# Performance work log

Measured on AMD Instinct MI355X. Metric: run time of the kernel, lower is better.

## Reference

```python
import jax, jax.numpy as jnp
import numpy as np
from jax.scipy.special import gammaln

REG = 0.1  # reg_param from __init__


def setup_inputs() -> dict:
    key = jax.random.key(0)
    k1, k2 = jax.random.split(key)
    D, C, S, Q = 512, 64, 16, 2048  # feature_dim, n_way, shots, n_query
    X_support = jax.random.normal(k1, (C * S, D), dtype=jnp.float32)
    # balanced class labels (equivalent to argmax of a one-hot y)
    labels = jnp.arange(C * S, dtype=jnp.int32) % C
    X_query = jax.random.normal(k2, (Q, D), dtype=jnp.float32)
    # learned parameters, initialized exactly as in the torch module
    m = jnp.zeros((1, D), dtype=jnp.float32)
    kappa = jnp.asarray(0.1, dtype=jnp.float32)
    nu = jnp.asarray(float(D), dtype=jnp.float32)
    triu_diag = jnp.ones((D,), dtype=jnp.float32)
    triu_lower = jnp.eye(D, dtype=jnp.float32)
    return {"X_support": X_support, "labels": labels, "X_query": X_query,
            "m": m, "kappa": kappa, "nu": nu,
            "triu_diag": triu_diag, "triu_lower": triu_lower, "n_classes": 64}


def _forward(X_support, X_query, m, kappa, nu, triu_diag, triu_lower, labels, n_classes):
    N, D = X_support.shape
    C = int(n_classes)
    S = N // C  # balanced episode: N_j == S for every class

    # lower_triu = diag(|triu_diag|) + triu_lower * strictly_lower_mask
    mask = jnp.tril(jnp.ones((D, D), dtype=X_support.dtype), -1)
    L = jnp.diag(jnp.abs(triu_diag)) + triu_lower * mask

    kap = jnp.abs(kappa) + 1e-6
    nu_ = jnp.clip(nu, D - 1 + 1e-6)

    # group support samples by class: [C, S, D] (stable sort keeps per-class order)
    order = jnp.argsort(labels)
    Xg = X_support[order].reshape(C, S, D)
    Xmean = Xg.mean(axis=1)  # [C, D]

    # posterior means mu_j = kappa/(kappa+N) m + N/(kappa+N) mean(X_j)
    mu = (kap / (kap + S)) * m + (S / (kap + S)) * Xmean  # [C, D]

    # sum_outer(X_j) as one batched GEMM instead of a per-row loop
    XtX = jnp.einsum('csd,cse->cde', Xg, Xg)  # [C, D, D]
    base = L @ L.T + kap * (m.T @ m)          # [D, D], shared across classes
    S_ns = base[None] + XtX - (kap + S) * jnp.einsum('cd,ce->cde', mu, mu)
    sigma = S_ns * ((kap + S + 1.0) / ((nu_ + S - D + 1.0) * (kap + S)))  # [C, D, D]

    eye = jnp.eye(D, dtype=sigma.dtype)
    sigma_inv = (1.0 - REG) * jnp.linalg.inv(sigma) + REG * eye  # regularize()

    common = nu_ + S + 1.0 - D  # scalar (equal shots per class)
    _, logdet = jnp.linalg.slogdet(sigma)  # [C]
    bias = (gammaln(0.5 * (common + D)) - gammaln(0.5 * common)
            - 0.5 * D * jnp.log(common) - 0.5 * logdet)  # [C]

    # batched Mahalanobis distances: replaces nested python loops in predict()
    diff = X_query[None, :, :] - mu[:, None, :]              # [C, Q, D]
    t = jnp.einsum('cqd,cde->cqe', diff, sigma_inv)          # [C, Q, D]
    dist = jnp.sum(t * diff, axis=-1)                        # [C, Q]

    logits = bias[:, None] - 0.5 * (common + D) * jnp.log1p(dist / common)
    return logits.T  # [Q, C]


def reference(X_support, labels, X_query, m, kappa, nu, triu_diag, triu_lower, n_classes):
    return _forward(X_support, X_query, m, kappa, nu, triu_diag, triu_lower,
                    labels, n_classes)
```

## Files before the change

### kernel.cpp

```cpp
#include <hip/hip_runtime.h>
#include <math.h>

#define DD    512
#define CNUM  64
#define SHOTS 16
#define NSUP  1024
#define QNQ   2048
#define REGP  0.1f
#define XKS   4

typedef __attribute__((ext_vector_type(8))) short short8;
typedef __attribute__((ext_vector_type(4))) float f32x4;

__device__ __forceinline__ unsigned short f2bf(float f) {
  unsigned int u = __float_as_uint(f);
  unsigned int r = (u + 0x7fffu + ((u >> 16) & 1u)) >> 16;
  return (unsigned short)r;
}
__device__ __forceinline__ float bf2f(unsigned short h) {
  return __uint_as_float((unsigned int)h << 16);
}

static constexpr size_t OFF_W     = 0;
static constexpr size_t OFF_MU    = OFF_W     + 512*512;
static constexpr size_t OFF_Y     = OFF_MU    + 64*512;
static constexpr size_t OFF_Z     = OFF_Y     + 3136*512;
static constexpr size_t OFF_WM    = OFF_Z     + 3136;
static constexpr size_t OFF_CONST = OFF_WM    + 512;
static constexpr size_t OFF_IDX   = OFF_CONST + 16;
static constexpr size_t OFF_RMAP  = OFF_IDX   + 1024;
static constexpr size_t OFF_ZG    = OFF_RMAP  + 1088;
static constexpr size_t OFF_VMU   = OFF_ZG    + 1088;
static constexpr size_t OFF_MUBMU = OFF_VMU   + 1088;
static constexpr size_t OFF_MUN   = OFF_MUBMU + 64;
static constexpr size_t OFF_MINV  = OFF_MUN   + 64;
static constexpr size_t OFF_BIAS  = OFF_MINV  + 64*289;
static constexpr size_t OFF_QNRM  = OFF_BIAS  + 64;
static constexpr size_t OFF_YN    = OFF_QNRM  + 2048;
static constexpr size_t OFF_XMU   = OFF_YN    + 2048;
static constexpr size_t OFF_RG    = OFF_XMU   + (size_t)XKS*2048*64;
static constexpr size_t OFF_P     = OFF_RG    + 1088*2048;
static constexpr size_t OFF_PX    = OFF_P     + 3136*512;
static constexpr size_t OFF_PW    = OFF_PX    + 3136*512;


__device__ __forceinline__ void px_rows(const float* __restrict__ Xq,
    const float* __restrict__ Xs, unsigned short* __restrict__ PX, int r0) {
  int tid = threadIdx.x;
  int row = r0 + (tid >> 6), lane = tid & 63;
  const float* src = (row < QNQ) ? Xq + (size_t)row * DD
                                 : Xs + (size_t)(row - QNQ) * DD;
  size_t prow = (size_t)row * 1024;
  #pragma unroll
  for (int p = 0; p < 2; p++) {
    int col = lane * 8 + p * 4;
    float4 v = *(const float4*)(src + col);
    ushort4 hi, lo;
    hi.x = f2bf(v.x); lo.x = f2bf(v.x - bf2f(hi.x));
    hi.y = f2bf(v.y); lo.y = f2bf(v.y - bf2f(hi.y));
    hi.z = f2bf(v.z); lo.z = f2bf(v.z - bf2f(hi.z));
    hi.w = f2bf(v.w); lo.w = f2bf(v.w - bf2f(hi.w));
    *(ushort4*)(PX + prow + col) = hi;
    *(ushort4*)(PX + prow + 512 + col) = lo;
  }
}

__global__ __launch_bounds__(256) void f_init(const float* tdiag, const float* tlow,
    const float* kappa, const float* nu, const int* labels, const float* Xs,
    const float* Xq, const float* m, float* W, float* cst, int* idx,
    int* rowmap, float* mu, float* mun,
    unsigned short* PX, unsigned short* PW) {
  __shared__ float sh[2 * 64 * 68 + 32 * 33];
  __shared__ int sidx[SHOTS];
  int b = blockIdx.x, tid = threadIdx.x;
  if (b < 8) {
    int jb = b;
    float* Ld = sh;
    float* Wd = sh + 64 * 68;
    float* tsh = sh + 2 * 64 * 68;
    for (int t = tid; t < 4096; t += 256) {
      int r = t >> 6, c = t & 63;
      int gr = jb * 64 + r;
      float v = (r == c) ? fabsf(tdiag[gr])
              : (r > c ? tlow[(size_t)gr * DD + jb * 64 + c] : 0.0f);
      Ld[r * 68 + c] = v;
      Wd[r * 68 + c] = 0.0f;
    }
    __syncthreads();
    if (tid < 64) {
      int s = tid >> 4, t = tid & 15;
      int r0 = s * 16;
      #pragma unroll
      for (int i = 0; i < 16; i++) {
        float w = (i == t) ? 1.0f : 0.0f;
        #pragma unroll
        for (int k = 0; k < 16; k++)
          if (k < i) w -= Ld[(r0 + i) * 68 + r0 + k] * Wd[(r0 + k) * 68 + r0 + t];
        Wd[(r0 + i) * 68 + r0 + t] = w / Ld[(r0 + i) * 68 + r0 + i];
      }
    }
    __syncthreads();
    for (int g2 = 0; g2 < 2; g2++) {
      int r0 = g2 * 32 + 16, c0 = g2 * 32;
      int rr = tid >> 4, cc = tid & 15;
      float t_ = 0.0f;
      #pragma unroll
      for (int k = 0; k < 16; k++)
        t_ += Ld[(r0 + rr) * 68 + c0 + k] * Wd[(c0 + k) * 68 + c0 + cc];
      tsh[rr * 33 + cc] = t_;
      __syncthreads();
      float x = 0.0f;
      #pragma unroll
      for (int k = 0; k < 16; k++)
        x -= Wd[(r0 + rr) * 68 + r0 + k] * tsh[k * 33 + cc];
      Wd[(r0 + rr) * 68 + c0 + cc] = x;
      __syncthreads();
    }
    {
      int rr = tid >> 6, cc = tid & 63;
      #pragma unroll
      for (int p = 0; p < 4; p++) {
        int r = rr + p * 4, c = cc;
        if (c < 32) {
          float t_ = 0.0f;
          #pragma unroll
          for (int k = 0; k < 32; k++)
            t_ += Ld[(32 + r) * 68 + k] * Wd[k * 68 + c];
          tsh[r * 33 + c] = t_;
        } else {
          int c2 = c - 32;
          float t_ = 0.0f;
          #pragma unroll
          for (int k = 0; k < 32; k++)
            t_ += Ld[(32 + r + 16) * 68 + k] * Wd[k * 68 + c2];
          tsh[(r + 16) * 33 + c2] = t_;
        }
      }
      __syncthreads();
      #pragma unroll
      for (int p = 0; p < 4; p++) {
        int r = rr + p * 4, c = cc;
        int r2 = (c < 32) ? r : r + 16;
        int c2 = (c < 32) ? c : c - 32;
        float x = 0.0f;
        #pragma unroll
        for (int k = 0; k < 32; k++)
          x -= Wd[(32 + r2) * 68 + 32 + k] * tsh[k * 33 + c2];
        Wd[(32 + r2) * 68 + c2] = x;
      }
    }
    __syncthreads();
    float* Wblk = W + (size_t)(jb * 64) * DD + jb * 64;
    for (int t = tid; t < 4096; t += 256) {
      int r = t >> 6, c = t & 63;
      float v = Wd[r * 68 + c];
      Wblk[(size_t)r * DD + c] = v;
      unsigned short h = f2bf(v), l = f2bf(v - bf2f(h));
      size_t prow = (size_t)(jb * 64 + r) * 1024 + jb * 64 + c;
      PW[prow] = h;
      PW[prow + 512] = l;
    }
  } else if (b == 8) {
    if (tid == 0) {
      float kap = fabsf(kappa[0]) + 1e-6f;
      float nu_ = fmaxf(nu[0], (float)(DD - 1) + 1e-6f);
      float common = nu_ + (float)SHOTS + 1.0f - (float)DD;
      float scale = (kap + SHOTS + 1.0f) / ((nu_ + SHOTS - DD + 1.0f) * (kap + SHOTS));
      cst[0] = kap;
      cst[1] = scale;
      cst[2] = common;
      cst[3] = 0.5f * (common + DD);
      cst[4] = lgammaf(0.5f * (common + DD)) - lgammaf(0.5f * common)
               - 0.5f * (float)DD * logf(common);
      cst[5] = -(kap + SHOTS);
      cst[6] = kap / (kap + SHOTS);
      cst[7] = 1.0f / (kap + SHOTS);
      cst[8] = (float)DD * logf(scale);
      cst[9] = -1.0f / (kap + SHOTS);
    }
  } else if (b < 73) {
    int c = b - 9;
    if (tid < 64) {
      int lane = tid, cnt = 0;
      for (int i0 = 0; i0 < NSUP; i0 += 64) {
        int lab = labels[i0 + lane];
        unsigned long long mm = __ballot(lab == c);
        if (lab == c) {
          int pos = cnt + __popcll(mm & ((1ull << lane) - 1ull));
          if (pos < SHOTS) idx[c * SHOTS + pos] = i0 + lane;
        }
        cnt += __popcll(mm);
      }
    }
    __syncthreads();
    if (tid < 17)
      rowmap[c * 17 + tid] = (tid < SHOTS) ? (QNQ + idx[c * SHOTS + tid])
                                           : (QNQ + NSUP + c);
  } else {
    int c = b - 73;
    if (tid < 64) {
      int lane = tid, cnt = 0;
      for (int i0 = 0; i0 < NSUP; i0 += 64) {
        int lab = labels[i0 + lane];
        unsigned long long mm = __ballot(lab == c);
        if (lab == c) {
          int pos = cnt + __popcll(mm & ((1ull << lane) - 1ull));
          if (pos < SHOTS) sidx[pos] = i0 + lane;
        }
        cnt += __popcll(mm);
      }
    }
    __syncthreads();
    float kap = fabsf(kappa[0]) + 1e-6f;
    float cm = kap / (kap + SHOTS), cx = 1.0f / (kap + SHOTS);
    float* red = sh;
    float acc = 0.0f;
    size_t prow = (size_t)(3072 + c) * 1024;
    for (int d = tid; d < DD; d += 256) {
      float s = 0.0f;
      for (int sh_ = 0; sh_ < SHOTS; sh_++)
        s += Xs[(size_t)sidx[sh_] * DD + d];
      float v = cm * m[d] + cx * s;
      mu[(size_t)c * DD + d] = v;
      unsigned short h = f2bf(v), l = f2bf(v - bf2f(h));
      PX[prow + d] = h;
      PX[prow + 512 + d] = l;
      acc += v * v;
    }
    red[tid] = acc;
    __syncthreads();
    for (int off = 128; off > 0; off >>= 1) {
      if (tid < off) red[tid] += red[tid + off];
      __syncthreads();
    }
    if (tid == 0) mun[c] = red[0];
  }
}

__device__ __forceinline__ void tile_stage(float* S, const float* __restrict__ G, int ldg) {
  int tid = threadIdx.x;
  #pragma unroll
  for (int p = 0; p < 4; p++) {
    int f4 = tid + 256 * p;
    int row = f4 >> 4, c4 = (f4 & 15) * 4;
    *(float4*)&S[row * 68 + c4] = *(const float4*)(G + (size_t)row * ldg + c4);
  }
}
__device__ __forceinline__ void tile_fma(float acc[4][4], const float* As, const float* Bs) {
  int tid = threadIdx.x, tr = tid >> 4, tc = tid & 15;
  #pragma unroll
  for (int kk = 0; kk < 64; kk++) {
    float a[4];
    #pragma unroll
    for (int x = 0; x < 4; x++) a[x] = As[(tr * 4 + x) * 68 + kk];
    float4 bv = *(const float4*)&Bs[kk * 68 + tc * 4];
    float bb[4] = {bv.x, bv.y, bv.z, bv.w};
    #pragma unroll
    for (int x = 0; x < 4; x++)
      #pragma unroll
      for (int y = 0; y < 4; y++) acc[x][y] += a[x] * bb[y];
  }
}
__device__ __forceinline__ void tile_out_neg(const float acc[4][4], float* W,
    unsigned short* PW, int gr0, int gc0) {
  int tid = threadIdx.x, tr = tid >> 4, tc = tid & 15;
  #pragma unroll
  for (int x = 0; x < 4; x++) {
    #pragma unroll
    for (int y = 0; y < 4; y++) {
      float v = -acc[x][y];
      W[(size_t)(gr0 + tr * 4 + x) * DD + gc0 + tc * 4 + y] = v;
      unsigned short h = f2bf(v), l = f2bf(v - bf2f(h));
      size_t prow = (size_t)(gr0 + tr * 4 + x) * 1024 + gc0 + tc * 4 + y;
      PW[prow] = h;
      PW[prow + 512] = l;
    }
  }
}

#define GBK 16
__global__ __launch_bounds__(256) void k_m128_xmu(const float* __restrict__ tlow,
    const float* __restrict__ W_, float* __restrict__ Wout,
    const float* __restrict__ Xq, const float* __restrict__ Mu,
    float* __restrict__ xmup, unsigned short* __restrict__ PW) {
  __shared__ float sh[3 * 64 * 68];
  int b = blockIdx.x, tid = threadIdx.x;
  if (b < 4) {
    float* As = sh;
    float* Bs = sh + 64 * 68;
    float* tsh = sh + 2 * 64 * 68;
    int base = b * 128;
    float tacc[4][4] = {};
    tile_stage(As, tlow + (size_t)(base + 64) * DD + base, DD);
    tile_stage(Bs, W_ + (size_t)base * DD + base, DD);
    __syncthreads();
    tile_fma(tacc, As, Bs);
    __syncthreads();
    {
      int tr = tid >> 4, tc = tid & 15;
      #pragma unroll
      for (int x = 0; x < 4; x++)
        #pragma unroll
        for (int y = 0; y < 4; y++) tsh[(tr * 4 + x) * 68 + tc * 4 + y] = tacc[x][y];
    }
    tile_stage(As, W_ + (size_t)(base + 64) * DD + base + 64, DD);
    __syncthreads();
    float xacc[4][4] = {};
    tile_fma(xacc, As, tsh);
    tile_out_neg(xacc, Wout, PW, base + 64, base);
  } else {
    float* Ms = sh;
    float* Qs = sh + 64 * 68;
    int xb = b - 4;
    int bm = (xb & 63) * 32, kq = xb >> 6;
    int tr = tid >> 4, tc = tid & 15;
    float acc[4][2] = {};
    int k0s = kq * (DD / XKS), k0e = k0s + DD / XKS;
    for (int k0 = k0s; k0 < k0e; k0 += GBK) {
      {
        int row = tid >> 2, k4 = tid & 3;
        float4 v = *(const float4*)(Mu + (size_t)row * DD + k0 + k4 * 4);
        Ms[(k4 * 4 + 0) * 68 + row] = v.x; Ms[(k4 * 4 + 1) * 68 + row] = v.y;
        Ms[(k4 * 4 + 2) * 68 + row] = v.z; Ms[(k4 * 4 + 3) * 68 + row] = v.w;
      }
      if (tid < 128) {
        int row = tid >> 2, k4 = tid & 3;
        float4 v = *(const float4*)(Xq + (size_t)(bm + row) * DD + k0 + k4 * 4);
        Qs[(k4 * 4 + 0) * 36 + row] = v.x; Qs[(k4 * 4 + 1) * 36 + row] = v.y;
        Qs[(k4 * 4 + 2) * 36 + row] = v.z; Qs[(k4 * 4 + 3) * 36 + row] = v.w;
      }
      __syncthreads();
      #pragma unroll
      for (int kk = 0; kk < GBK; kk++) {
        float4 m0 = *(const float4*)&Ms[kk * 68 + tr * 4];
        float a[4] = {m0.x, m0.y, m0.z, m0.w};
        float q0 = Qs[kk * 36 + tc * 2], q1 = Qs[kk * 36 + tc * 2 + 1];
        #pragma unroll
        for (int y = 0; y < 4; y++) {
          acc[y][0] += a[y] * q0;
          acc[y][1] += a[y] * q1;
        }
      }
      __syncthreads();
    }
    #pragma unroll
    for (int y = 0; y < 4; y++) {
      float2 v = make_float2(acc[y][0], acc[y][1]);
      *(float2*)(xmup + ((size_t)kq * CNUM + tr * 4 + y) * QNQ + bm + tc * 2) = v;
    }
  }
}

__global__ __launch_bounds__(256) void k_m256(const float* __restrict__ tlow,
    float* __restrict__ W, unsigned short* __restrict__ PW,
    const float* __restrict__ Xq, const float* __restrict__ Xs,
    unsigned short* __restrict__ PX) {
  __shared__ float sh[3 * 64 * 68];
  int b = blockIdx.x, tid = threadIdx.x;
  if (b >= 8) { px_rows(Xq, Xs, PX, (b - 8) * 4); return; }
  float* As = sh;
  float* Bs = sh + 64 * 68;
  float* tsh = sh + 2 * 64 * 68;
  int g = b >> 2, rem = b & 3, i = rem >> 1, j = rem & 1;
  int base = g * 256;
  float xacc[4][4] = {};
  for (int k = 0; k <= i; k++) {
    float tacc[4][4] = {};
    for (int l = j; l < 2; l++) {
      __syncthreads();
      tile_stage(As, tlow + (size_t)(base + 128 + 64 * k) * DD + base + 64 * l, DD);
      tile_stage(Bs, W + (size_t)(base + 64 * l) * DD + base + 64 * j, DD);
      __syncthreads();
      tile_fma(tacc, As, Bs);
    }
    __syncthreads();
    {
      int tr = tid >> 4, tc = tid & 15;
      #pragma unroll
      for (int x = 0; x < 4; x++)
        #pragma unroll
        for (int y = 0; y < 4; y++) tsh[(tr * 4 + x) * 68 + tc * 4 + y] = tacc[x][y];
    }
    tile_stage(As, W + (size_t)(base + 128 + 64 * i) * DD + base + 128 + 64 * k, DD);
    __syncthreads();
    tile_fma(xacc, As, tsh);
  }
  tile_out_neg(xacc, W, PW, base + 128 + 64 * i, base + 64 * j);
}

__device__ __forceinline__ void nn64_sh(float* As, float* Bs,
    const float* __restrict__ A, int lda, const float* __restrict__ B, int ldb,
    float* __restrict__ Cd, int ldc, int k0, int k1, float sgn,
    unsigned short* __restrict__ Pw, int gr0, int gc0) {
  int tid = threadIdx.x, tr = tid >> 4, tc = tid & 15;
  float acc[4][4] = {};
  for (int kc = k0; kc < k1; kc += 64) {
    #pragma unroll
    for (int p = 0; p < 4; p++) {
      int f4 = tid + 256 * p;
      int row = f4 >> 4, c4 = f4 & 15;
      *(float4*)&As[row * 68 + c4 * 4] = *(const float4*)(A + (size_t)row * lda + kc + c4 * 4);
      *(float4*)&Bs[row * 68 + c4 * 4] = *(const float4*)(B + (size_t)(kc + row) * ldb + c4 * 4);
    }
    __syncthreads();
    #pragma unroll
    for (int kk = 0; kk < 64; kk++) {
      float a[4];
      #pragma unroll
      for (int x = 0; x < 4; x++) a[x] = As[(tr * 4 + x) * 68 + kk];
      float4 bv = *(const float4*)&Bs[kk * 68 + tc * 4];
      float bb[4] = {bv.x, bv.y, bv.z, bv.w};
      #pragma unroll
      for (int x = 0; x < 4; x++)
        #pragma unroll
        for (int y = 0; y < 4; y++) acc[x][y] += a[x] * bb[y];
    }
    __syncthreads();
  }
  #pragma unroll
  for (int x = 0; x < 4; x++) {
    float4 v = make_float4(sgn * acc[x][0], sgn * acc[x][1],
                           sgn * acc[x][2], sgn * acc[x][3]);
    *(float4*)(Cd + (size_t)(tr * 4 + x) * ldc + tc * 4) = v;
    if (Pw) {
      size_t prow = (size_t)(gr0 + tr * 4 + x) * 1024 + gc0 + tc * 4;
      float vv[4] = {v.x, v.y, v.z, v.w};
      #pragma unroll
      for (int y = 0; y < 4; y++) {
        unsigned short h = f2bf(vv[y]), l = f2bf(vv[y] - bf2f(h));
        Pw[prow + y] = h;
        Pw[prow + 512 + y] = l;
      }
    }
  }
}

__global__ __launch_bounds__(256) void k_triT(const float* __restrict__ tlow,
                                              const float* __restrict__ W,
                                              float* __restrict__ T,
                                              const float* __restrict__ Xq,
                                              const float* __restrict__ Xs,
                                              unsigned short* __restrict__ PX) {
  __shared__ float sh[2 * 64 * 68];
  int b = blockIdx.x;
  if (b >= 16) { px_rows(Xq, Xs, PX, 1024 + (b - 16) * 4); return; }
  int ti = b >> 2, tj = b & 3;
  const float* A = tlow + (size_t)(256 + ti * 64) * DD;
  const float* B = W + (size_t)tj * 64;
  float* Cd = T + (size_t)(ti * 64) * 256 + tj * 64;
  nn64_sh(sh, sh + 64 * 68, A, DD, B, DD, Cd, 256, tj * 64, 256, 1.0f, nullptr, 0, 0);
}

__global__ __launch_bounds__(256) void k_triX(float* __restrict__ W,
                                              const float* __restrict__ T,
                                              unsigned short* __restrict__ PW,
                                              const float* __restrict__ Xq,
                                              const float* __restrict__ Xs,
                                              unsigned short* __restrict__ PX) {
  __shared__ float sh[2 * 64 * 68];
  int b = blockIdx.x;
  if (b >= 16) { px_rows(Xq, Xs, PX, 2048 + (b - 16) * 4); return; }
  int ti = b >> 2, tj = b & 3;
  const float* A = W + (size_t)(256 + ti * 64) * DD + 256;
  const float* B = T + tj * 64;
  int gr0 = 256 + ti * 64, gc0 = tj * 64;
  float* Cd = W + (size_t)gr0 * DD + gc0;
  nn64_sh(sh, sh + 64 * 68, A, DD, B, 256, Cd, DD, 0, (ti + 1) * 64, -1.0f, PW, gr0, gc0);
}

#define PSTR 72
__global__ __launch_bounds__(256) void f_y_wm(const unsigned short* __restrict__ PX,
    const unsigned short* __restrict__ PW, const float* __restrict__ W,
    const float* __restrict__ m, float* __restrict__ Y,
    unsigned short* __restrict__ Pm, float* __restrict__ wm) {
  __shared__ unsigned short AshH[64 * PSTR];
  __shared__ unsigned short AshL[64 * PSTR];
  __shared__ unsigned short BshH[64 * PSTR];
  __shared__ unsigned short BshL[64 * PSTR];
  int b = blockIdx.x, tid = threadIdx.x;
  if (b < 392) {
    int mt = b >> 3, nt = b & 7;
    int bm = mt * 64, bn = nt * 64;
    int lane = tid & 63, wave = tid >> 6;
    int wr = wave >> 1, wc = wave & 1;
    int mrow = lane & 15, q = lane >> 4;
    f32x4 acc00 = {}, acc01 = {}, acc10 = {}, acc11 = {};
    int kchunks = nt + 1;
    for (int it = 0; it < kchunks; it++) {
      int kc = it * 64;
      #pragma unroll
      for (int p = 0; p < 2; p++) {
        int idx = tid + 256 * p;
        int row = idx >> 3, c8 = (idx & 7) * 8;
        *(short8*)&AshH[row * PSTR + c8] =
            *(const short8*)(PX + (size_t)(bm + row) * 1024 + kc + c8);
        *(short8*)&AshL[row * PSTR + c8] =
            *(const short8*)(PX + (size_t)(bm + row) * 1024 + 512 + kc + c8);
        *(short8*)&BshH[row * PSTR + c8] =
            *(const short8*)(PW + (size_t)(bn + row) * 1024 + kc + c8);
        *(short8*)&BshL[row * PSTR + c8] =
            *(const short8*)(PW + (size_t)(bn + row) * 1024 + 512 + kc + c8);
      }
      __syncthreads();
      #pragma unroll
      for (int ks = 0; ks < 2; ks++) {
        int ko = ks * 32 + q * 8;
        short8 ah0 = *(const short8*)&AshH[(wr * 32 + mrow) * PSTR + ko];
        short8 ah1 = *(const short8*)&AshH[(wr * 32 + 16 + mrow) * PSTR + ko];
        short8 al0 = *(const short8*)&AshL[(wr * 32 + mrow) * PSTR + ko];
        short8 al1 = *(const short8*)&AshL[(wr * 32 + 16 + mrow) * PSTR + ko];
        short8 bh0 = *(const short8*)&BshH[(wc * 32 + mrow) * PSTR + ko];
        short8 bh1 = *(const short8*)&BshH[(wc * 32 + 16 + mrow) * PSTR + ko];
        short8 bl0 = *(const short8*)&BshL[(wc * 32 + mrow) * PSTR + ko];
        short8 bl1 = *(const short8*)&BshL[(wc * 32 + 16 + mrow) * PSTR + ko];
        acc00 = __builtin_amdgcn_mfma_f32_16x16x32_bf16(ah0, bh0, acc00, 0, 0, 0);
        acc00 = __builtin_amdgcn_mfma_f32_16x16x32_bf16(ah0, bl0, acc00, 0, 0, 0);
        acc00 = __builtin_amdgcn_mfma_f32_16x16x32_bf16(al0, bh0, acc00, 0, 0, 0);
        acc01 = __builtin_amdgcn_mfma_f32_16x16x32_bf16(ah0, bh1, acc01, 0, 0, 0);
        acc01 = __builtin_amdgcn_mfma_f32_16x16x32_bf16(ah0, bl1, acc01, 0, 0, 0);
        acc01 = __builtin_amdgcn_mfma_f32_16x16x32_bf16(al0, bh1, acc01, 0, 0, 0);
        acc10 = __builtin_amdgcn_mfma_f32_16x16x32_bf16(ah1, bh0, acc10, 0, 0, 0);
        acc10 = __builtin_amdgcn_mfma_f32_16x16x32_bf16(ah1, bl0, acc10, 0, 0, 0);
        acc10 = __builtin_amdgcn_mfma_f32_16x16x32_bf16(al1, bh0, acc10, 0, 0, 0);
        acc11 = __builtin_amdgcn_mfma_f32_16x16x32_bf16(ah1, bh1, acc11, 0, 0, 0);
        acc11 = __builtin_amdgcn_mfma_f32_16x16x32_bf16(ah1, bl1, acc11, 0, 0, 0);
        acc11 = __builtin_amdgcn_mfma_f32_16x16x32_bf16(al1, bh1, acc11, 0, 0, 0);
      }
      __syncthreads();
    }
    #pragma unroll
    for (int r = 0; r < 4; r++) {
      int row0 = bm + wr * 32 + q * 4 + r;
      int row1 = row0 + 16;
      int col0 = bn + wc * 32 + mrow;
      float vv[4] = {acc00[r], acc01[r], acc10[r], acc11[r]};
      int rows[4] = {row0, row0, row1, row1};
      int cols[4] = {col0, col0 + 16, col0, col0 + 16};
      #pragma unroll
      for (int e = 0; e < 4; e++) {
        Y[(size_t)rows[e] * DD + cols[e]] = vv[e];
        unsigned short h = f2bf(vv[e]), l = f2bf(vv[e] - bf2f(h));
        Pm[(size_t)rows[e] * 1024 + cols[e]] = h;
        Pm[(size_t)rows[e] * 1024 + 512 + cols[e]] = l;
      }
    }
  } else {
    int wave = tid >> 6, lane = tid & 63;
    int row = (b - 392) * 4 + wave;
    float s = 0.0f;
    for (int j = lane; j <= row; j += 64) s += W[(size_t)row * DD + j] * m[j];
    for (int off = 32; off > 0; off >>= 1) s += __shfl_down(s, off);
    if (lane == 0) wm[row] = s;
  }
}

__global__ __launch_bounds__(256) void f_z_rg_gram(const unsigned short* __restrict__ Pm,
    const float* __restrict__ Y, const float* __restrict__ tdiag,
    const int* __restrict__ rowmap, const float* __restrict__ Xq,
    const float* __restrict__ wm, float* __restrict__ cst,
    float* __restrict__ Rg,
    float* __restrict__ z, float* __restrict__ qn, float* __restrict__ yn,
    float* __restrict__ zg, float* __restrict__ Vmu, float* __restrict__ muBmu,
    float* __restrict__ Minv, float* __restrict__ bias) {
  __shared__ float sh[9216];
  __shared__ float csmS;
  int b = blockIdx.x, tid = threadIdx.x;
  if (b < 64) {
    int c = b;
    int lane = tid & 63, wave = tid >> 6;
    float* Ys  = sh;
    float* aug = sh + 8772;
    float* zsv = aug + 306;
    float kap = cst[0], cst9 = cst[9];
    for (int t = tid; t < 17 * 128; t += 256) {
      int r = t >> 7, col = t & 127;
      *(float4*)&Ys[r * 516 + col * 4] =
          *(const float4*)(Y + (size_t)rowmap[c * 17 + r] * DD + col * 4);
    }
    float ldb_r = 0.0f;
    if (wave == 0) {
      float aa = 0.0f, ll = 0.0f;
      for (int t = lane; t < DD; t += 64) {
        float w = wm[t]; aa += w * w;
        ll += logf(fabsf(tdiag[t]));
      }
      #pragma unroll
      for (int off = 32; off > 0; off >>= 1) {
        aa += __shfl_xor(aa, off);
        ll += __shfl_xor(ll, off);
      }
      ldb_r = 2.0f * ll + logf(1.0f + kap * aa);
      if (lane == 0) csmS = kap / (1.0f + kap * aa);
    }
    __syncthreads();
    if (wave > 0) {
      for (int a = wave - 1; a < 17; a += 3) {
        float s = 0.0f;
        for (int j = lane; j < 128; j += 64) {
          float4 yv = *(const float4*)&Ys[a * 516 + j * 4];
          float4 wv = *(const float4*)(wm + j * 4);
          s += yv.x * wv.x + yv.y * wv.y + yv.z * wv.z + yv.w * wv.w;
        }
        #pragma unroll
        for (int off = 32; off > 0; off >>= 1) s += __shfl_xor(s, off);
        if (lane == 0) zsv[a] = s;
      }
    }
    __syncthreads();
    float csm = csmS;
    for (int e = tid; e < 153; e += 256) {
      int a = (int)((sqrtf(8.0f * (float)e + 1.0f) - 1.0f) * 0.5f);
      while (((a + 1) * (a + 2)) / 2 <= e) a++;
      while ((a * (a + 1)) / 2 > e) a--;
      int bb = e - (a * (a + 1)) / 2;
      const float* ra = &Ys[a * 516];
      const float* rb = &Ys[bb * 516];
      float s = 0.0f;
      for (int k = 0; k < 128; k++) {
        float4 va = *(const float4*)&ra[k * 4];
        float4 vb = *(const float4*)&rb[k * 4];
        s += va.x * vb.x + va.y * vb.y + va.z * vb.z + va.w * vb.w;
      }
      float g = s - csm * zsv[a] * zsv[bb];
      if (a == bb) g += (a < 16) ? 1.0f : cst9;
      aug[a * 18 + bb] = g;
      if (a != bb) aug[bb * 18 + a] = g;
    }
    __syncthreads();
    if (wave == 0) {
      float colv[17];
      bool left = lane < 17;
      bool right = (lane >= 17 && lane < 34);
      #pragma unroll
      for (int r = 0; r < 17; r++) {
        float lv = aug[r * 18 + (lane & 31)];
        colv[r] = left ? lv : ((right && (lane - 17) == r) ? 1.0f : 0.0f);
      }
      float det = 0.0f;
      #pragma unroll
      for (int k = 0; k < 17; k++) {
        float best = fabsf(colv[k]); int bp = k;
        #pragma unroll
        for (int r = k + 1; r < 17; r++) {
          float v = fabsf(colv[r]);
          if (v > best) { best = v; bp = r; }
        }
        int p = __shfl(bp, k);
        float pv = colv[k];
        #pragma unroll
        for (int r = k + 1; r < 17; r++) pv = (p == r) ? colv[r] : pv;
        float oldk = colv[k];
        #pragma unroll
        for (int r = k + 1; r < 17; r++) colv[r] = (p == r) ? oldk : colv[r];
        colv[k] = pv;
        float piv = __shfl(pv, k);
        if (lane == 0) det += logf(fabsf(piv));
        float invp = 1.0f / piv;
        float rk = pv * invp;
        colv[k] = rk;
        #pragma unroll
        for (int r = 0; r < 17; r++) {
          if (r == k) continue;
          float ck = __shfl(colv[r], k);
          colv[r] = fmaf(-ck, rk, colv[r]);
        }
      }
      if (right) {
        int bb = lane - 17;
        #pragma unroll
        for (int r = 0; r < 17; r++)
          Minv[(size_t)c * 289 + r * 17 + bb] = colv[r];
      }
      if (lane == 0) {
        float slog = logf(fabsf(cst[5])) + det;
        float logdetSigma = cst[8] + ldb_r + slog;
        bias[c] = cst[4] - 0.5f * logdetSigma;
      }
    } else if (wave == 1) {
      if (lane < 17) {
        float gv = aug[lane * 18 + 16];
        if (lane == 16) gv -= cst9;
        Vmu[c * 17 + lane] = gv;
        if (lane == 16) muBmu[c] = gv;
        zg[c * 17 + lane] = zsv[lane];
      }
    }
  } else if (b == 64) {
    if (tid < 64) {
      float aa = 0.0f, ll = 0.0f;
      for (int t = tid; t < DD; t += 64) {
        float w = wm[t]; aa += w * w;
        ll += logf(fabsf(tdiag[t]));
      }
      #pragma unroll
      for (int off = 32; off > 0; off >>= 1) {
        aa += __shfl_xor(aa, off);
        ll += __shfl_xor(ll, off);
      }
      if (tid == 0) {
        float kap = cst[0];
        cst[10] = kap / (1.0f + kap * aa);
        cst[11] = 2.0f * ll + logf(1.0f + kap * aa);
      }
    }
  } else if (b < 609) {
    unsigned short* ush = (unsigned short*)sh;
    unsigned short* AH = ush;
    unsigned short* AL = ush + 64 * PSTR;
    unsigned short* BH = ush + 2 * 64 * PSTR;
    unsigned short* BL = ush + 3 * 64 * PSTR;
    int rb = b - 65;
    int bm = (rb >> 5) * 64, bn = (rb & 31) * 64;
    int lane = tid & 63, wave = tid >> 6;
    int wr = wave >> 1, wc = wave & 1;
    int mrow = lane & 15, q = lane >> 4;
    int srowA[2];
    #pragma unroll
    for (int p = 0; p < 2; p++) srowA[p] = rowmap[bm + ((tid + 256 * p) >> 3)];
    f32x4 acc00 = {}, acc01 = {}, acc10 = {}, acc11 = {};
    for (int it = 0; it < 8; it++) {
      int kc = it * 64;
      #pragma unroll
      for (int p = 0; p < 2; p++) {
        int idx = tid + 256 * p;
        int row = idx >> 3, c8 = (idx & 7) * 8;
        *(short8*)&AH[row * PSTR + c8] =
            *(const short8*)(Pm + (size_t)srowA[p] * 1024 + kc + c8);
        *(short8*)&AL[row * PSTR + c8] =
            *(const short8*)(Pm + (size_t)srowA[p] * 1024 + 512 + kc + c8);
        *(short8*)&BH[row * PSTR + c8] =
            *(const short8*)(Pm + (size_t)(bn + row) * 1024 + kc + c8);
        *(short8*)&BL[row * PSTR + c8] =
            *(const short8*)(Pm + (size_t)(bn + row) * 1024 + 512 + kc + c8);
      }
      __syncthreads();
      #pragma unroll
      for (int ks = 0; ks < 2; ks++) {
        int ko = ks * 32 + q * 8;
        short8 ah0 = *(const short8*)&AH[(wr * 32 + mrow) * PSTR + ko];
        short8 ah1 = *(const short8*)&AH[(wr * 32 + 16 + mrow) * PSTR + ko];
        short8 al0 = *(const short8*)&AL[(wr * 32 + mrow) * PSTR + ko];
        short8 al1 = *(const short8*)&AL[(wr * 32 + 16 + mrow) * PSTR + ko];
        short8 bh0 = *(const short8*)&BH[(wc * 32 + mrow) * PSTR + ko];
        short8 bh1 = *(const short8*)&BH[(wc * 32 + 16 + mrow) * PSTR + ko];
        short8 bl0 = *(const short8*)&BL[(wc * 32 + mrow) * PSTR + ko];
        short8 bl1 = *(const short8*)&BL[(wc * 32 + 16 + mrow) * PSTR + ko];
        acc00 = __builtin_amdgcn_mfma_f32_16x16x32_bf16(ah0, bh0, acc00, 0, 0, 0);
        acc00 = __builtin_amdgcn_mfma_f32_16x16x32_bf16(ah0, bl0, acc00, 0, 0, 0);
        acc00 = __builtin_amdgcn_mfma_f32_16x16x32_bf16(al0, bh0, acc00, 0, 0, 0);
        acc01 = __builtin_amdgcn_mfma_f32_16x16x32_bf16(ah0, bh1, acc01, 0, 0, 0);
        acc01 = __builtin_amdgcn_mfma_f32_16x16x32_bf16(ah0, bl1, acc01, 0, 0, 0);
        acc01 = __builtin_amdgcn_mfma_f32_16x16x32_bf16(al0, bh1, acc01, 0, 0, 0);
        acc10 = __builtin_amdgcn_mfma_f32_16x16x32_bf16(ah1, bh0, acc10, 0, 0, 0);
        acc10 = __builtin_amdgcn_mfma_f32_16x16x32_bf16(ah1, bl0, acc10, 0, 0, 0);
        acc10 = __builtin_amdgcn_mfma_f32_16x16x32_bf16(al1, bh0, acc10, 0, 0, 0);
        acc11 = __builtin_amdgcn_mfma_f32_16x16x32_bf16(ah1, bh1, acc11, 0, 0, 0);
        acc11 = __builtin_amdgcn_mfma_f32_16x16x32_bf16(ah1, bl1, acc11, 0, 0, 0);
        acc11 = __builtin_amdgcn_mfma_f32_16x16x32_bf16(al1, bh1, acc11, 0, 0, 0);
      }
      __syncthreads();
    }
    #pragma unroll
    for (int r = 0; r < 4; r++) {
      int row0 = bm + wr * 32 + q * 4 + r;
      int row1 = row0 + 16;
      int col0 = bn + wc * 32 + mrow;
      Rg[(size_t)row0 * QNQ + col0]      = acc00[r];
      Rg[(size_t)row0 * QNQ + col0 + 16] = acc01[r];
      Rg[(size_t)row1 * QNQ + col0]      = acc10[r];
      Rg[(size_t)row1 * QNQ + col0 + 16] = acc11[r];
    }
  } else {
    int wave = tid >> 6, lane = tid & 63;
    int row = (b - 609) * 4 + wave;
    const float* xr = Xq + (size_t)row * DD;
    const float* yr = Y + (size_t)row * DD;
    float sz = 0.0f, s1 = 0.0f, s2 = 0.0f;
    for (int j4 = lane; j4 < 128; j4 += 64) {
      float4 xv = *(const float4*)(xr + j4 * 4);
      float4 yv = *(const float4*)(yr + j4 * 4);
      float4 wv = *(const float4*)(wm + j4 * 4);
      sz += yv.x * wv.x + yv.y * wv.y + yv.z * wv.z + yv.w * wv.w;
      s1 += xv.x * xv.x + xv.y * xv.y + xv.z * xv.z + xv.w * xv.w;
      s2 += yv.x * yv.x + yv.y * yv.y + yv.z * yv.z + yv.w * yv.w;
    }
    for (int off = 32; off > 0; off >>= 1) {
      sz += __shfl_down(sz, off);
      s1 += __shfl_down(s1, off);
      s2 += __shfl_down(s2, off);
    }
    if (lane == 0) {
      z[row] = sz;
      qn[row] = s1;
      yn[row] = s2;
    }
  }
}

__global__ __launch_bounds__(256) void k_logits(const float* __restrict__ Rg,
    const float* z, const float* zg,
    const float* Vmu, const float* muBmu, const float* mun, const float* yn,
    const float* qn, const float* xmup, const float* Minv, const float* bias,
    const float* cst, float* out) {
  __shared__ float Ms[289], Vs[17], Zs[17];
  int c = blockIdx.y;
  int q = blockIdx.x * 256 + threadIdx.x;
  for (int t = threadIdx.x; t < 289; t += 256) Ms[t] = Minv[(size_t)c * 289 + t];
  if (threadIdx.x < 17) {
    Vs[threadIdx.x] = Vmu[c * 17 + threadIdx.x];
    Zs[threadIdx.x] = zg[c * 17 + threadIdx.x];
  }
  __syncthreads();
  float csm = cst[10], scale = cst[1], common = cst[2], coef = cst[3];
  float zq = z[q];
  float r[17];
  float xBmu = 0.0f;
  for (int a = 0; a < 17; a++) {
    float raw = Rg[(size_t)(c * 17 + a) * QNQ + q] - csm * Zs[a] * zq;
    if (a == 16) xBmu = raw;
    r[a] = raw - Vs[a];
  }
  float qB = yn[q] - csm * zq * zq;
  float quadB = qB - 2.0f * xBmu + muBmu[c];
  float corr = 0.0f;
  for (int a = 0; a < 17; a++) {
    float e = 0.0f;
    for (int bb = 0; bb < 17; bb++) e += Ms[a * 17 + bb] * r[bb];
    corr += r[a] * e;
  }
  float distB = (quadB - corr) / scale;
  float xm = 0.0f;
  #pragma unroll
  for (int p = 0; p < XKS; p++)
    xm += xmup[((size_t)(p * CNUM + c)) * QNQ + q];
  float dn = qn[q] - 2.0f * xm + mun[c];
  float dist = (1.0f - REGP) * distB + REGP * dn;
  out[(size_t)q * CNUM + c] = bias[c] - coef * log1pf(dist / common);
}

extern "C" void kernel_launch(void* const* d_in, const int* in_sizes, int n_in,
                              void* d_out, int out_size, void* d_ws, size_t ws_size,
                              hipStream_t stream) {
  const float* Xs    = (const float*)d_in[0];
  const int*   labels= (const int*)d_in[1];
  const float* Xq    = (const float*)d_in[2];
  const float* m     = (const float*)d_in[3];
  const float* kappa = (const float*)d_in[4];
  const float* nu    = (const float*)d_in[5];
  const float* tdiag = (const float*)d_in[6];
  const float* tlow  = (const float*)d_in[7];
  float* ws = (float*)d_ws;
  float* W    = ws + OFF_W;
  float* mu   = ws + OFF_MU;
  float* Y    = ws + OFF_Y;
  float* z    = ws + OFF_Z;
  float* wm   = ws + OFF_WM;
  float* cst  = ws + OFF_CONST;
  int*   idx  = (int*)(ws + OFF_IDX);
  int*   rmap = (int*)(ws + OFF_RMAP);
  float* zg   = ws + OFF_ZG;
  float* Vmu  = ws + OFF_VMU;
  float* muBmu= ws + OFF_MUBMU;
  float* mun  = ws + OFF_MUN;
  float* Minv = ws + OFF_MINV;
  float* bias = ws + OFF_BIAS;
  float* qn   = ws + OFF_QNRM;
  float* yn   = ws + OFF_YN;
  float* xmup = ws + OFF_XMU;
  float* Rg   = ws + OFF_RG;
  unsigned short* P  = (unsigned short*)(ws + OFF_P);
  unsigned short* PX = (unsigned short*)(ws + OFF_PX);
  unsigned short* PW = (unsigned short*)(ws + OFF_PW);
  float* Ttmp = ws + OFF_RG;
  float* out  = (float*)d_out;

  f_init<<<137, 256, 0, stream>>>(tdiag, tlow, kappa, nu, labels, Xs, Xq, m,
                                  W, cst, idx, rmap, mu, mun, PX, PW);
  k_m128_xmu<<<260, 256, 0, stream>>>(tlow, W, W, Xq, mu, xmup, PW);
  k_m256<<<8 + 256, 256, 0, stream>>>(tlow, W, PW, Xq, Xs, PX);
  k_triT<<<16 + 256, 256, 0, stream>>>(tlow, W, Ttmp, Xq, Xs, PX);
  k_triX<<<16 + 256, 256, 0, stream>>>(W, Ttmp, PW, Xq, Xs, PX);
  f_y_wm<<<520, 256, 0, stream>>>(PX, PW, W, m, Y, P, wm);
  f_z_rg_gram<<<64 + 1 + 544 + 512, 256, 0, stream>>>(P, Y, tdiag, rmap, Xq, wm,
                                                      cst, Rg, z, qn, yn,
                                                      zg, Vmu, muBmu, Minv, bias);
  k_logits<<<dim3(QNQ / 256, CNUM), 256, 0, stream>>>(Rg, z, zg, Vmu, muBmu,
                                                      mun, yn, qn, xmup, Minv, bias,
                                                      cst, out);
  (void)in_sizes; (void)n_in; (void)out_size; (void)ws_size;
}
```

Measured before the change: 187.5 us.

## Fuse two-pass triangular inverse block update into one kernel, widen xmu K-tile

The two kernels that computed the 256x256 off-diagonal block of the triangular inverse (first T = L21*W11 into a scratch buffer, then W21 = -W22*T) become one kernel. Each block now recomputes the needed T tiles in shared memory and accumulates the product directly. This removes a launch and the global round trip through the temporary, at the cost of redundant T-tile computation across blocks. The diff also keeps the 16x16 forward-substitution column in registers instead of shared memory, and doubles the K step of the query-mean product to cut loop iterations and barriers.

```diff
diff --git a/kernel.cpp b/kernel.cpp
--- a/kernel.cpp
+++ b/kernel.cpp
@@ -90,14 +90,17 @@
     if (tid < 64) {
       int s = tid >> 4, t = tid & 15;
       int r0 = s * 16;
+      float wreg[16];
       #pragma unroll
       for (int i = 0; i < 16; i++) {
         float w = (i == t) ? 1.0f : 0.0f;
         #pragma unroll
         for (int k = 0; k < 16; k++)
-          if (k < i) w -= Ld[(r0 + i) * 68 + r0 + k] * Wd[(r0 + k) * 68 + r0 + t];
-        Wd[(r0 + i) * 68 + r0 + t] = w / Ld[(r0 + i) * 68 + r0 + i];
-      }
+          if (k < i) w -= Ld[(r0 + i) * 68 + r0 + k] * wreg[k];
+        wreg[i] = w / Ld[(r0 + i) * 68 + r0 + i];
+      }
+      #pragma unroll
+      for (int i = 0; i < 16; i++) Wd[(r0 + i) * 68 + r0 + t] = wreg[i];
     }
     __syncthreads();
     for (int g2 = 0; g2 < 2; g2++) {
@@ -278,7 +281,7 @@
   }
 }
 
-#define GBK 16
+#define GBK 32
 __global__ __launch_bounds__(256) void k_m128_xmu(const float* __restrict__ tlow,
     const float* __restrict__ W_, float* __restrict__ Wout,
     const float* __restrict__ Xq, const float* __restrict__ Mu,
@@ -317,14 +320,16 @@
     float acc[4][2] = {};
     int k0s = kq * (DD / XKS), k0e = k0s + DD / XKS;
     for (int k0 = k0s; k0 < k0e; k0 += GBK) {
-      {
-        int row = tid >> 2, k4 = tid & 3;
+      #pragma unroll
+      for (int p = 0; p < 2; p++) {
+        int idx = tid + 256 * p;
+        int row = idx >> 3, k4 = idx & 7;
         float4 v = *(const float4*)(Mu + (size_t)row * DD + k0 + k4 * 4);
         Ms[(k4 * 4 + 0) * 68 + row] = v.x; Ms[(k4 * 4 + 1) * 68 + row] = v.y;
         Ms[(k4 * 4 + 2) * 68 + row] = v.z; Ms[(k4 * 4 + 3) * 68 + row] = v.w;
       }
-      if (tid < 128) {
-        int row = tid >> 2, k4 = tid & 3;
+      {
+        int row = tid >> 3, k4 = tid & 7;
         float4 v = *(const float4*)(Xq + (size_t)(bm + row) * DD + k0 + k4 * 4);
         Qs[(k4 * 4 + 0) * 36 + row] = v.x; Qs[(k4 * 4 + 1) * 36 + row] = v.y;
         Qs[(k4 * 4 + 2) * 36 + row] = v.z; Qs[(k4 * 4 + 3) * 36 + row] = v.w;
@@ -388,84 +393,40 @@
   tile_out_neg(xacc, W, PW, base + 128 + 64 * i, base + 64 * j);
 }
 
-__device__ __forceinline__ void nn64_sh(float* As, float* Bs,
-    const float* __restrict__ A, int lda, const float* __restrict__ B, int ldb,
-    float* __restrict__ Cd, int ldc, int k0, int k1, float sgn,
-    unsigned short* __restrict__ Pw, int gr0, int gc0) {
-  int tid = threadIdx.x, tr = tid >> 4, tc = tid & 15;
-  float acc[4][4] = {};
-  for (int kc = k0; kc < k1; kc += 64) {
-    #pragma unroll
-    for (int p = 0; p < 4; p++) {
-      int f4 = tid + 256 * p;
-      int row = f4 >> 4, c4 = f4 & 15;
-      *(float4*)&As[row * 68 + c4 * 4] = *(const float4*)(A + (size_t)row * lda + kc + c4 * 4);
-      *(float4*)&Bs[row * 68 + c4 * 4] = *(const float4*)(B + (size_t)(kc + row) * ldb + c4 * 4);
-    }
-    __syncthreads();
-    #pragma unroll
-    for (int kk = 0; kk < 64; kk++) {
-      float a[4];
-      #pragma unroll
-      for (int x = 0; x < 4; x++) a[x] = As[(tr * 4 + x) * 68 + kk];
-      float4 bv = *(const float4*)&Bs[kk * 68 + tc * 4];
-      float bb[4] = {bv.x, bv.y, bv.z, bv.w};
+__global__ __launch_bounds__(256) void k_tri512(const float* __restrict__ tlow,
+    float* __restrict__ W, unsigned short* __restrict__ PW,
+    const float* __restrict__ Xq, const float* __restrict__ Xs,
+    unsigned short* __restrict__ PX) {
+  __shared__ float sh[3 * 64 * 68];
+  int b = blockIdx.x, tid = threadIdx.x;
+  if (b >= 16) { px_rows(Xq, Xs, PX, 1024 + (b - 16) * 4); return; }
+  float* As = sh;
+  float* Bs = sh + 64 * 68;
+  float* tsh = sh + 2 * 64 * 68;
+  int ti = b >> 2, tj = b & 3;
+  float xacc[4][4] = {};
+  for (int k = 0; k <= ti; k++) {
+    float tacc[4][4] = {};
+    for (int l = tj; l < 4; l++) {
+      __syncthreads();
+      tile_stage(As, tlow + (size_t)(256 + k * 64) * DD + l * 64, DD);
+      tile_stage(Bs, W + (size_t)(l * 64) * DD + tj * 64, DD);
+      __syncthreads();
+      tile_fma(tacc, As, Bs);
+    }
+    __syncthreads();
+    {
+      int tr = tid >> 4, tc = tid & 15;
       #pragma unroll
       for (int x = 0; x < 4; x++)
         #pragma unroll
-        for (int y = 0; y < 4; y++) acc[x][y] += a[x] * bb[y];
-    }
-    __syncthreads();
-  }
-  #pragma unroll
-  for (int x = 0; x < 4; x++) {
-    float4 v = make_float4(sgn * acc[x][0], sgn * acc[x][1],
-                           sgn * acc[x][2], sgn * acc[x][3]);
-    *(float4*)(Cd + (size_t)(tr * 4 + x) * ldc + tc * 4) = v;
-    if (Pw) {
-      size_t prow = (size_t)(gr0 + tr * 4 + x) * 1024 + gc0 + tc * 4;
-      float vv[4] = {v.x, v.y, v.z, v.w};
-      #pragma unroll
-      for (int y = 0; y < 4; y++) {
-        unsigned short h = f2bf(vv[y]), l = f2bf(vv[y] - bf2f(h));
-        Pw[prow + y] = h;
-        Pw[prow + 512 + y] = l;
-      }
-    }
-  }
-}
-
-__global__ __launch_bounds__(256) void k_triT(const float* __restrict__ tlow,
-                                              const float* __restrict__ W,
-                                              float* __restrict__ T,
-                                              const float* __restrict__ Xq,
-                                              const float* __restrict__ Xs,
-                                              unsigned short* __restrict__ PX) {
-  __shared__ float sh[2 * 64 * 68];
-  int b = blockIdx.x;
-  if (b >= 16) { px_rows(Xq, Xs, PX, 1024 + (b - 16) * 4); return; }
-  int ti = b >> 2, tj = b & 3;
-  const float* A = tlow + (size_t)(256 + ti * 64) * DD;
-  const float* B = W + (size_t)tj * 64;
-  float* Cd = T + (size_t)(ti * 64) * 256 + tj * 64;
-  nn64_sh(sh, sh + 64 * 68, A, DD, B, DD, Cd, 256, tj * 64, 256, 1.0f, nullptr, 0, 0);
-}
-
-__global__ __launch_bounds__(256) void k_triX(float* __restrict__ W,
-                                              const float* __restrict__ T,
-                                              unsigned short* __restrict__ PW,
-                                              const float* __restrict__ Xq,
-                                              const float* __restrict__ Xs,
-                                              unsigned short* __restrict__ PX) {
-  __shared__ float sh[2 * 64 * 68];
-  int b = blockIdx.x;
-  if (b >= 16) { px_rows(Xq, Xs, PX, 2048 + (b - 16) * 4); return; }
-  int ti = b >> 2, tj = b & 3;
-  const float* A = W + (size_t)(256 + ti * 64) * DD + 256;
-  const float* B = T + tj * 64;
-  int gr0 = 256 + ti * 64, gc0 = tj * 64;
-  float* Cd = W + (size_t)gr0 * DD + gc0;
-  nn64_sh(sh, sh + 64 * 68, A, DD, B, 256, Cd, DD, 0, (ti + 1) * 64, -1.0f, PW, gr0, gc0);
+        for (int y = 0; y < 4; y++) tsh[(tr * 4 + x) * 68 + tc * 4 + y] = tacc[x][y];
+    }
+    tile_stage(As, W + (size_t)(256 + ti * 64) * DD + 256 + k * 64, DD);
+    __syncthreads();
+    tile_fma(xacc, As, tsh);
+  }
+  tile_out_neg(xacc, W, PW, 256 + ti * 64, tj * 64);
 }
 
 #define PSTR 72
@@ -871,15 +832,13 @@
   unsigned short* P  = (unsigned short*)(ws + OFF_P);
   unsigned short* PX = (unsigned short*)(ws + OFF_PX);
   unsigned short* PW = (unsigned short*)(ws + OFF_PW);
-  float* Ttmp = ws + OFF_RG;
   float* out  = (float*)d_out;
 
   f_init<<<137, 256, 0, stream>>>(tdiag, tlow, kappa, nu, labels, Xs, Xq, m,
                                   W, cst, idx, rmap, mu, mun, PX, PW);
   k_m128_xmu<<<260, 256, 0, stream>>>(tlow, W, W, Xq, mu, xmup, PW);
   k_m256<<<8 + 256, 256, 0, stream>>>(tlow, W, PW, Xq, Xs, PX);
-  k_triT<<<16 + 256, 256, 0, stream>>>(tlow, W, Ttmp, Xq, Xs, PX);
-  k_triX<<<16 + 256, 256, 0, stream>>>(W, Ttmp, PW, Xq, Xs, PX);
+  k_tri512<<<16 + 512, 256, 0, stream>>>(tlow, W, PW, Xq, Xs, PX);
   f_y_wm<<<520, 256, 0, stream>>>(PX, PW, W, m, Y, P, wm);
   f_z_rg_gram<<<64 + 1 + 544 + 512, 256, 0, stream>>>(P, Y, tdiag, rmap, Xq, wm,
                                                       cst, Rg, z, qn, yn,
```

Measured after the change: 211.6 us. 12.8% more time.
